# Kernel optimization log

Measured on AMD Instinct MI355X. Metric: run time of the kernel, lower is better.

The kernel has to match this reference:

```python
import jax, jax.numpy as jnp
import numpy as np

DIM = 64
WIDTH = 128
INPUT_DIM = 16
N_NODES = 50000
N_EDGES = 100000
N_GRAPHS = 2500
STEPS = 5


def setup_inputs() -> dict:
    key = jax.random.key(0)
    ks = jax.random.split(key, 24)
    d = DIM
    def nrm(i, shape, fan_in):
        return jax.random.normal(ks[i], shape, jnp.float32) / np.float32(np.sqrt(fan_in))
    return {
        "x": jax.random.normal(ks[0], (N_NODES, INPUT_DIM - 1), jnp.float32),
        "z": jax.random.normal(ks[1], (N_NODES,), jnp.float32),
        "edge_attr": jax.random.uniform(ks[2], (N_EDGES, 5), jnp.float32),
        "lin0_w": nrm(3, (INPUT_DIM, d), INPUT_DIM),
        "lin0_b": jnp.zeros((d,), jnp.float32),
        "emlp_w1": nrm(4, (5, WIDTH), 5),
        "emlp_b1": jnp.zeros((WIDTH,), jnp.float32),
        "emlp_w2": nrm(5, (WIDTH, d * d), WIDTH),
        "emlp_b2": jnp.zeros((d * d,), jnp.float32),
        "conv_root": nrm(6, (d, d), d),
        "conv_bias": jnp.zeros((d,), jnp.float32),
        "gru_wi": nrm(7, (3 * d, d), d),
        "gru_wh": nrm(8, (3 * d, d), d),
        "gru_bi": jnp.zeros((3 * d,), jnp.float32),
        "gru_bh": jnp.zeros((3 * d,), jnp.float32),
        "lstm_wi": nrm(9, (4 * d, 2 * d), 2 * d),
        "lstm_wh": nrm(10, (4 * d, d), d),
        "lstm_bi": jnp.zeros((4 * d,), jnp.float32),
        "lstm_bh": jnp.zeros((4 * d,), jnp.float32),
        "lin1_w": nrm(11, (2 * d, d), 2 * d),
        "lin1_b": jnp.zeros((d,), jnp.float32),
        "lin2_w": nrm(12, (d, 1), d),
        "lin2_b": jnp.zeros((1,), jnp.float32),
        "edge_index": jax.random.randint(ks[13], (2, N_EDGES), 0, N_NODES),
        "batch": jnp.sort(jax.random.randint(ks[14], (N_NODES,), 0, N_GRAPHS)),
        "num_graphs": N_GRAPHS,
    }


def reference(x, z, edge_attr, lin0_w, lin0_b, emlp_w1, emlp_b1, emlp_w2, emlp_b2,
              conv_root, conv_bias, gru_wi, gru_wh, gru_bi, gru_bh,
              lstm_wi, lstm_wh, lstm_bi, lstm_bh, lin1_w, lin1_b, lin2_w, lin2_b,
              edge_index, batch, num_graphs):
    d = lin0_w.shape[1]
    n = x.shape[0]
    src, dst = edge_index[0], edge_index[1]
    # lin0 on [x | z]
    out = jax.nn.relu(jnp.concatenate([x, z[:, None]], axis=-1) @ lin0_w + lin0_b)  # [N, d]
    h = out
    # edge MLP -> per-edge weight matrix [E, d, d] (edge_attr fixed, compute once)
    ew = (jax.nn.relu(edge_attr @ emlp_w1 + emlp_b1) @ emlp_w2 + emlp_b2).reshape(-1, d, d)
    deg = jax.ops.segment_sum(jnp.ones_like(src, jnp.float32), dst, num_segments=n)
    denom = jnp.maximum(deg, 1.0)[:, None]
    for _ in range(STEPS):
        # NNConv: gather-matmul-scatter(mean) + root transform + bias
        msg = jnp.einsum('ei,eio->eo', out[src], ew)  # [E, d]
        aggr = jax.ops.segment_sum(msg, dst, num_segments=n) / denom
        m = jax.nn.relu(aggr + out @ conv_root + conv_bias)
        # GRU cell (torch gate order r, z, n)
        gi = m @ gru_wi.T + gru_bi
        gh = h @ gru_wh.T + gru_bh
        i_r, i_z, i_n = jnp.split(gi, 3, axis=-1)
        h_r, h_z, h_n = jnp.split(gh, 3, axis=-1)
        r = jax.nn.sigmoid(i_r + h_r)
        zg = jax.nn.sigmoid(i_z + h_z)
        ng = jnp.tanh(i_n + r * h_n)
        h = (1.0 - zg) * ng + zg * h
        out = h
    # Set2Set pooling (LSTM(2d -> d), torch gate order i, f, g, o)
    B = num_graphs
    q_star = jnp.zeros((B, 2 * d), out.dtype)
    hh = jnp.zeros((B, d), out.dtype)
    cc = jnp.zeros((B, d), out.dtype)
    for _ in range(STEPS):
        g = q_star @ lstm_wi.T + lstm_bi + hh @ lstm_wh.T + lstm_bh
        gi_, gf_, gg_, go_ = jnp.split(g, 4, axis=-1)
        cc = jax.nn.sigmoid(gf_) * cc + jax.nn.sigmoid(gi_) * jnp.tanh(gg_)
        hh = jax.nn.sigmoid(go_) * jnp.tanh(cc)
        q = hh
        e = jnp.sum(out * q[batch], axis=-1)  # [N]
        emax = jax.ops.segment_max(e, batch, num_segments=B)
        a = jnp.exp(e - emax[batch])
        asum = jax.ops.segment_sum(a, batch, num_segments=B) + 1e-16
        a = a / asum[batch]
        r_pool = jax.ops.segment_sum(a[:, None] * out, batch, num_segments=B)  # [B, d]
        q_star = jnp.concatenate([q, r_pool], axis=-1)
    y = jax.nn.relu(q_star @ lin1_w + lin1_b) @ lin2_w + lin2_b
    return y.reshape(-1)
```

## Files before the change

### kernel.cpp

```cpp
#include <hip/hip_runtime.h>
#include <hip/hip_bf16.h>

#define NN 50000
#define NE 100000
#define NG 2500
#define WW 128
#define EPAD 100096
#define KCH 264

typedef _Float16 h8 __attribute__((ext_vector_type(8)));
typedef _Float16 h4 __attribute__((ext_vector_type(4)));
typedef float    f4 __attribute__((ext_vector_type(4)));

#define GLOAD_LDS16(g, l) __builtin_amdgcn_global_load_lds( \
    (const __attribute__((address_space(1))) void*)(g),     \
    (__attribute__((address_space(3))) void*)(l), 16, 0, 0)

__device__ __forceinline__ float sigf(float x) { return 1.0f / (1.0f + __expf(-x)); }

__global__ void k_zero4(float4* __restrict__ p, int n4) {
    int i = blockIdx.x * 256 + threadIdx.x;
    if (i < n4) p[i] = make_float4(0.f, 0.f, 0.f, 0.f);
}

__global__ void k_transpose(float* dst, const float* src, int rows, int cols) {
    int idx = blockIdx.x * 256 + threadIdx.x;
    if (idx >= rows * cols) return;
    int r = idx / cols, c = idx % cols;
    dst[c * rows + r] = src[idx];
}

__global__ void k_lin0(const float* __restrict__ x, const float* __restrict__ z,
                       const float* __restrict__ w, const float* __restrict__ b,
                       float* __restrict__ s) {
    int idx = blockIdx.x * 256 + threadIdx.x;
    int n = idx >> 6, o = idx & 63;
    float acc = b[o];
#pragma unroll
    for (int i = 0; i < 15; i++) acc += x[n * 15 + i] * w[i * 64 + o];
    acc += z[n] * w[15 * 64 + o];
    s[idx] = fmaxf(acc, 0.0f);
}

__global__ void k_deg(const int* __restrict__ dstI, float* __restrict__ deg) {
    int e = blockIdx.x * 256 + threadIdx.x;
    if (e < NE) atomicAdd(&deg[dstI[e]], 1.0f);
}

__global__ void k_s16(const float* __restrict__ s, _Float16* __restrict__ s16) {
    int i = blockIdx.x * 256 + threadIdx.x;
    float4 v = ((const float4*)s)[i];
    h4 o = { (_Float16)v.x, (_Float16)v.y, (_Float16)v.z, (_Float16)v.w };
    *((h4*)s16 + i) = o;
}

__global__ void k_gstart(const int* __restrict__ batch, int* __restrict__ gstart) {
    int n = blockIdx.x * 256 + threadIdx.x;
    if (n > NN) return;
    int b1 = (n < NN) ? batch[n] : NG;
    int b0 = (n == 0) ? -1 : batch[n - 1];
    for (int g = b0 + 1; g <= b1; g++) gstart[g] = n;
}

__global__ void k_emlp_t(const float* __restrict__ ea, const float* __restrict__ w1,
                         const float* __restrict__ b1, _Float16* __restrict__ hidT4) {
    __shared__ _Float16 hl[132][64];
    int t = threadIdx.x;
    int e0 = blockIdx.x * 64;
    int e_l = t & 63, w = t >> 6;
    int e = e0 + e_l;
    float a0 = 0, a1 = 0, a2 = 0, a3 = 0, a4 = 0;
    if (e < NE) {
        a0 = ea[e * 5 + 0]; a1 = ea[e * 5 + 1]; a2 = ea[e * 5 + 2];
        a3 = ea[e * 5 + 3]; a4 = ea[e * 5 + 4];
    }
    for (int h = w * 32; h < w * 32 + 32; h++) {
        float acc = b1[h];
        acc += a0 * w1[0 * 128 + h] + a1 * w1[1 * 128 + h] + a2 * w1[2 * 128 + h]
             + a3 * w1[3 * 128 + h] + a4 * w1[4 * 128 + h];
        hl[h][e_l] = (_Float16)fmaxf(acc, 0.0f);
    }
    if (t < 64) hl[128][t] = (_Float16)1.0f;
    else if (t < 128) hl[129][t - 64] = (_Float16)0.0f;
    else if (t < 192) hl[130][t - 128] = (_Float16)0.0f;
    else hl[131][t - 192] = (_Float16)0.0f;
    __syncthreads();
#pragma unroll
    for (int it = 0; it < 9; it++) {
        int hq = it * 4 + w;
        if (hq < 33) {
            h4 v = { hl[hq * 4 + 0][e_l], hl[hq * 4 + 1][e_l],
                     hl[hq * 4 + 2][e_l], hl[hq * 4 + 3][e_l] };
            *(h4*)(hidT4 + ((size_t)hq * EPAD + e0 + e_l) * 4) = v;
        }
    }
}

__global__ void k_prep_B(const float* __restrict__ w2, const float* __restrict__ b2,
                         _Float16* __restrict__ Bp) {
    int g = blockIdx.x * 256 + threadIdx.x;
    int l = g & 63, tt = (g >> 6) & 3, c = g >> 8;
    int n = tt * 16 + (l & 15);
    int kb = c * 32 + (l >> 4) * 8;
    h8 v;
#pragma unroll
    for (int j = 0; j < 8; j++) {
        int k = kb + j;
        float f = 0.0f;
        if (k < 8192) f = w2[(size_t)k * 64 + n];
        else if (k < 8256) f = b2[(k - 8192) * 64 + n];
        v[j] = (_Float16)f;
    }
    *((h8*)Bp + g) = v;
}

__global__ void k_prep_W(const float* __restrict__ conv_root,
                         const float* __restrict__ gru_wi,
                         const float* __restrict__ gru_wh,
                         _Float16* __restrict__ Bw) {
    int g = blockIdx.x * 256 + threadIdx.x;
    if (g >= 56 * 64) return;
    int l = g & 63, unit = g >> 6;
    int kb = ((unit & 1) * 32) + (l >> 4) * 8;
    h8 v;
    if (unit < 8) {
        int nt = unit >> 1;
        int n = nt * 16 + (l & 15);
#pragma unroll
        for (int j = 0; j < 8; j++) v[j] = (_Float16)conv_root[(kb + j) * 64 + n];
    } else if (unit < 32) {
        int nt = (unit - 8) >> 1;
        int o = nt * 16 + (l & 15);
#pragma unroll
        for (int j = 0; j < 8; j++) v[j] = (_Float16)gru_wi[o * 64 + kb + j];
    } else {
        int nt = (unit - 32) >> 1;
        int o = nt * 16 + (l & 15);
#pragma unroll
        for (int j = 0; j < 8; j++) v[j] = (_Float16)gru_wh[o * 64 + kb + j];
    }
    *((h8*)Bw + g) = v;
}

#define COMPUTE_PHASE(BUF, PAIR)                                               \
    _Pragma("unroll")                                                          \
    for (int c2 = 0; c2 < 4; c2++) {                                           \
        h8 b0 = *(const h8*)&Bl[BUF][(c2 * 4 + 0) * 64 + lane];                \
        h8 b1 = *(const h8*)&Bl[BUF][(c2 * 4 + 1) * 64 + lane];                \
        h8 b2 = *(const h8*)&Bl[BUF][(c2 * 4 + 2) * 64 + lane];                \
        h8 b3 = *(const h8*)&Bl[BUF][(c2 * 4 + 3) * 64 + lane];                \
        _Pragma("unroll")                                                      \
        for (int mt = 0; mt < 4; mt++) {                                       \
            h8 a = sA[mt][c2 & 1] * hfA[mt][(PAIR) * 2 + (c2 >> 1)];           \
            acc[mt][0] = __builtin_amdgcn_mfma_f32_16x16x32_f16(a, b0, acc[mt][0], 0, 0, 0); \
            acc[mt][1] = __builtin_amdgcn_mfma_f32_16x16x32_f16(a, b1, acc[mt][1], 0, 0, 0); \
            acc[mt][2] = __builtin_amdgcn_mfma_f32_16x16x32_f16(a, b2, acc[mt][2], 0, 0, 0); \
            acc[mt][3] = __builtin_amdgcn_mfma_f32_16x16x32_f16(a, b3, acc[mt][3], 0, 0, 0); \
        }                                                                      \
    }

__global__ __launch_bounds__(128, 2) void k_fused(
        const _Float16* __restrict__ s16, const _Float16* __restrict__ hidT4,
        const _Float16* __restrict__ Bp, const int* __restrict__ srcI,
        const int* __restrict__ dstI, float* __restrict__ aggr) {
    __shared__ uint4 Bl[2][1024];
    int t = threadIdx.x, w = t >> 6, lane = t & 63;
    int m = lane & 15, q = lane >> 4;
    int e_blk = blockIdx.x * 128;
    int ew0 = e_blk + w * 64;

    h8 sA[4][2];
#pragma unroll
    for (int mt = 0; mt < 4; mt++) {
        int e = ew0 + mt * 16 + m;
        int src = (e < NE) ? srcI[e] : 0;
        const _Float16* sp = s16 + (size_t)src * 64;
        sA[mt][0] = *(const h8*)(sp + q * 8);
        sA[mt][1] = *(const h8*)(sp + 32 + q * 8);
    }
    f4 acc[4][4];
#pragma unroll
    for (int mt = 0; mt < 4; mt++)
#pragma unroll
        for (int nt = 0; nt < 4; nt++) acc[mt][nt] = (f4){0.f, 0.f, 0.f, 0.f};

    const h4* hT = (const h4*)hidT4;
    h4 hfA[4], hfB[4];
#pragma unroll
    for (int mt = 0; mt < 4; mt++)
        hfA[mt] = hT[(size_t)0 * EPAD + ew0 + mt * 16 + m];

    {
        const uint4* bs = (const uint4*)Bp;
#pragma unroll
        for (int r = 0; r < 8; r++) {
            int idx = r * 128 + t;
            GLOAD_LDS16(bs + idx, &Bl[0][idx]);
        }
    }
    __syncthreads();

    for (int tt = 0; tt < 33; tt++) {
        {
            const uint4* bs = (const uint4*)Bp + (size_t)(2 * tt + 1) * 1024;
#pragma unroll
            for (int r = 0; r < 8; r++) {
                int idx = r * 128 + t;
                GLOAD_LDS16(bs + idx, &Bl[1][idx]);
            }
        }
        if (tt + 1 < 33) {
#pragma unroll
            for (int mt = 0; mt < 4; mt++)
                hfB[mt] = hT[(size_t)(tt + 1) * EPAD + ew0 + mt * 16 + m];
        }
        COMPUTE_PHASE(0, 0)
        __syncthreads();

        if (tt + 1 < 33) {
            const uint4* bs = (const uint4*)Bp + (size_t)(2 * tt + 2) * 1024;
#pragma unroll
            for (int r = 0; r < 8; r++) {
                int idx = r * 128 + t;
                GLOAD_LDS16(bs + idx, &Bl[0][idx]);
            }
        }
        COMPUTE_PHASE(1, 1)
        if (tt + 1 < 33) {
#pragma unroll
            for (int mt = 0; mt < 4; mt++) hfA[mt] = hfB[mt];
        }
        __syncthreads();
    }

#pragma unroll
    for (int mt = 0; mt < 4; mt++) {
        int eb = ew0 + mt * 16 + q * 4;
#pragma unroll
        for (int r = 0; r < 4; r++) {
            int e = eb + r;
            if (e < NE) {
                int d = dstI[e];
                float* ap = aggr + (size_t)d * 64 + m;
                atomicAdd(ap + 0,  acc[mt][0][r]);
                atomicAdd(ap + 16, acc[mt][1][r]);
                atomicAdd(ap + 32, acc[mt][2][r]);
                atomicAdd(ap + 48, acc[mt][3][r]);
            }
        }
    }
}

__global__ __launch_bounds__(256) void k_combine2(
        float* __restrict__ s, _Float16* __restrict__ s16,
        const float* __restrict__ aggr, const float* __restrict__ deg,
        const _Float16* __restrict__ Bw, const float* __restrict__ cb,
        const float* __restrict__ bi, const float* __restrict__ bh) {
    __shared__ _Float16 ml[4][16][72];
    int t = threadIdx.x, w = t >> 6, lane = t & 63;
    int m = lane & 15, q = lane >> 4;
    int nb = blockIdx.x * 64 + w * 16;

    h8 sa0, sa1;
    {
        int node = nb + m; if (node >= NN) node = NN - 1;
        const _Float16* sp = s16 + (size_t)node * 64;
        sa0 = *(const h8*)(sp + q * 8);
        sa1 = *(const h8*)(sp + 32 + q * 8);
    }
    const h8* BW = (const h8*)Bw;

    f4 X[4], GH[12];
#pragma unroll
    for (int nt = 0; nt < 4; nt++) {
        X[nt] = (f4){0.f, 0.f, 0.f, 0.f};
        X[nt] = __builtin_amdgcn_mfma_f32_16x16x32_f16(sa0, BW[(nt * 2 + 0) * 64 + lane], X[nt], 0, 0, 0);
        X[nt] = __builtin_amdgcn_mfma_f32_16x16x32_f16(sa1, BW[(nt * 2 + 1) * 64 + lane], X[nt], 0, 0, 0);
    }
#pragma unroll
    for (int nt = 0; nt < 12; nt++) {
        GH[nt] = (f4){0.f, 0.f, 0.f, 0.f};
        GH[nt] = __builtin_amdgcn_mfma_f32_16x16x32_f16(sa0, BW[(32 + nt * 2 + 0) * 64 + lane], GH[nt], 0, 0, 0);
        GH[nt] = __builtin_amdgcn_mfma_f32_16x16x32_f16(sa1, BW[(32 + nt * 2 + 1) * 64 + lane], GH[nt], 0, 0, 0);
    }
#pragma unroll
    for (int r = 0; r < 4; r++) {
        int node = nb + q * 4 + r; if (node >= NN) node = NN - 1;
        float dn = fmaxf(deg[node], 1.0f);
#pragma unroll
        for (int nt = 0; nt < 4; nt++) {
            int o = nt * 16 + m;
            float mv = X[nt][r] + aggr[(size_t)node * 64 + o] / dn + cb[o];
            ml[w][q * 4 + r][o] = (_Float16)fmaxf(mv, 0.0f);
        }
    }
    __syncthreads();
    h8 ma0 = *(const h8*)&ml[w][m][q * 8];
    h8 ma1 = *(const h8*)&ml[w][m][32 + q * 8];

    f4 GI[12];
#pragma unroll
    for (int nt = 0; nt < 12; nt++) {
        GI[nt] = (f4){0.f, 0.f, 0.f, 0.f};
        GI[nt] = __builtin_amdgcn_mfma_f32_16x16x32_f16(ma0, BW[(8 + nt * 2 + 0) * 64 + lane], GI[nt], 0, 0, 0);
        GI[nt] = __builtin_amdgcn_mfma_f32_16x16x32_f16(ma1, BW[(8 + nt * 2 + 1) * 64 + lane], GI[nt], 0, 0, 0);
    }
#pragma unroll
    for (int og = 0; og < 4; og++) {
        int o = og * 16 + m;
        float bir = bi[o],       bhr = bh[o];
        float biz = bi[64 + o],  bhz = bh[64 + o];
        float bin = bi[128 + o], bhn = bh[128 + o];
#pragma unroll
        for (int r = 0; r < 4; r++) {
            int node = nb + q * 4 + r;
            if (node >= NN) continue;
            float rr = sigf(GI[og][r] + bir + GH[og][r] + bhr);
            float zz = sigf(GI[4 + og][r] + biz + GH[4 + og][r] + bhz);
            float ng = tanhf(GI[8 + og][r] + bin + rr * (GH[8 + og][r] + bhn));
            float hold = s[(size_t)node * 64 + o];
            float hnew = (1.0f - zz) * ng + zz * hold;
            s[(size_t)node * 64 + o] = hnew;
            s16[(size_t)node * 64 + o] = (_Float16)hnew;
        }
    }
}

__global__ void k_s2s(float* __restrict__ q_star, float* __restrict__ hh,
                      float* __restrict__ cc, const float* __restrict__ LiT,
                      const float* __restrict__ LhT, const float* __restrict__ bi,
                      const float* __restrict__ bh, const float* __restrict__ s,
                      const int* __restrict__ gstart, float* __restrict__ e_v) {
    __shared__ float qs[128], hv[64], g[256], qn[64];
    int b = blockIdx.x, t = threadIdx.x;
    if (t < 128) qs[t] = q_star[b * 128 + t];
    else if (t < 192) hv[t - 128] = hh[b * 64 + t - 128];
    __syncthreads();
    float acc = bi[t] + bh[t];
    for (int k = 0; k < 128; k++) acc += qs[k] * LiT[k * 256 + t];
    for (int k = 0; k < 64; k++) acc += hv[k] * LhT[k * 256 + t];
    g[t] = acc;
    __syncthreads();
    if (t < 64) {
        float c_new = sigf(g[64 + t]) * cc[b * 64 + t] + sigf(g[t]) * tanhf(g[128 + t]);
        cc[b * 64 + t] = c_new;
        float hq = sigf(g[192 + t]) * tanhf(c_new);
        hh[b * 64 + t] = hq;
        qn[t] = hq;
        q_star[b * 128 + t] = hq;
    }
    __syncthreads();
    if (t >= 64) return;
    int o = t;
    int n0 = gstart[b], n1 = gstart[b + 1];
    float q = qn[o];
    float mx = -3.4e38f;
    for (int n = n0; n < n1; n++) {
        float v = s[(size_t)n * 64 + o] * q;
#pragma unroll
        for (int off = 32; off; off >>= 1) v += __shfl_xor(v, off, 64);
        if (o == 0) e_v[n] = v;
        mx = fmaxf(mx, v);
    }
    float asum = 0.0f, rp = 0.0f;
    for (int n = n0; n < n1; n++) {
        float a = __expf(e_v[n] - mx);
        asum += a;
        rp += a * s[(size_t)n * 64 + o];
    }
    q_star[b * 128 + 64 + o] = rp / (asum + 1e-16f);
}

__global__ void k_final(const float* __restrict__ q_star, const float* __restrict__ w1,
                        const float* __restrict__ b1, const float* __restrict__ w2,
                        const float* __restrict__ b2, float* __restrict__ y) {
    __shared__ float qs[128];
    int b = blockIdx.x, t = threadIdx.x;
    qs[t] = q_star[b * 128 + t];
    qs[64 + t] = q_star[b * 128 + 64 + t];
    __syncthreads();
    float acc = b1[t];
    for (int k = 0; k < 128; k++) acc += qs[k] * w1[k * 64 + t];
    float hid = fmaxf(acc, 0.0f) * w2[t];
#pragma unroll
    for (int off = 32; off; off >>= 1) hid += __shfl_down(hid, off, 64);
    if (t == 0) y[b] = hid + b2[0];
}

static inline void zero_f(float* p, size_t nfloats, hipStream_t stream) {
    int n4 = (int)(nfloats / 4);
    k_zero4<<<(n4 + 255) / 256, 256, 0, stream>>>((float4*)p, n4);
}

extern "C" void kernel_launch(void* const* d_in, const int* in_sizes, int n_in,
                              void* d_out, int out_size, void* d_ws, size_t ws_size,
                              hipStream_t stream) {
    const float* x       = (const float*)d_in[0];
    const float* z       = (const float*)d_in[1];
    const float* ea      = (const float*)d_in[2];
    const float* lin0_w  = (const float*)d_in[3];
    const float* lin0_b  = (const float*)d_in[4];
    const float* emlp_w1 = (const float*)d_in[5];
    const float* emlp_b1 = (const float*)d_in[6];
    const float* emlp_w2 = (const float*)d_in[7];
    const float* emlp_b2 = (const float*)d_in[8];
    const float* conv_r  = (const float*)d_in[9];
    const float* conv_b  = (const float*)d_in[10];
    const float* gru_wi  = (const float*)d_in[11];
    const float* gru_wh  = (const float*)d_in[12];
    const float* gru_bi  = (const float*)d_in[13];
    const float* gru_bh  = (const float*)d_in[14];
    const float* lstm_wi = (const float*)d_in[15];
    const float* lstm_wh = (const float*)d_in[16];
    const float* lstm_bi = (const float*)d_in[17];
    const float* lstm_bh = (const float*)d_in[18];
    const float* lin1_w  = (const float*)d_in[19];
    const float* lin1_b  = (const float*)d_in[20];
    const float* lin2_w  = (const float*)d_in[21];
    const float* lin2_b  = (const float*)d_in[22];
    const int* eidx      = (const int*)d_in[23];
    const int* batch     = (const int*)d_in[24];
    const int* srcI = eidx;
    const int* dstI = eidx + NE;
    float* y = (float*)d_out;

    char* w = (char*)d_ws;
    size_t off = 0;
    auto alloc = [&](size_t bytes) -> void* {
        void* p = w + off;
        off += (bytes + 255) & ~(size_t)255;
        return p;
    };
    float* s      = (float*)alloc((size_t)NN * 64 * 4);
    float* aggr   = (float*)alloc((size_t)NN * 64 * 4);
    float* deg    = (float*)alloc((size_t)NN * 4);
    float* e_v    = (float*)alloc((size_t)NN * 4);
    float* q_star = (float*)alloc((size_t)NG * 128 * 4);
    float* hh     = (float*)alloc((size_t)NG * 64 * 4);
    float* cc     = (float*)alloc((size_t)NG * 64 * 4);
    float* LiT    = (float*)alloc(256 * 128 * 4);
    float* LhT    = (float*)alloc(256 * 64 * 4);
    int*   gstart = (int*)alloc((size_t)(NG + 1) * 4);
    _Float16* s16 = (_Float16*)alloc((size_t)NN * 64 * 2);
    _Float16* hidT= (_Float16*)alloc((size_t)33 * EPAD * 4 * 2);
    _Float16* Bp  = (_Float16*)alloc((size_t)KCH * 4 * 64 * 8 * 2);
    _Float16* Bw  = (_Float16*)alloc((size_t)56 * 64 * 8 * 2);
    (void)ws_size;

    k_transpose<<<(256 * 128 + 255) / 256, 256, 0, stream>>>(LiT, lstm_wi, 256, 128);
    k_transpose<<<(256 * 64 + 255) / 256, 256, 0, stream>>>(LhT, lstm_wh, 256, 64);
    k_prep_W<<<14, 256, 0, stream>>>(conv_r, gru_wi, gru_wh, Bw);

    k_lin0<<<NN * 64 / 256, 256, 0, stream>>>(x, z, lin0_w, lin0_b, s);
    k_s16<<<NN * 16 / 256, 256, 0, stream>>>(s, s16);
    zero_f(deg, NN, stream);
    k_deg<<<(NE + 255) / 256, 256, 0, stream>>>(dstI, deg);
    k_gstart<<<(NN + 256) / 256, 256, 0, stream>>>(batch, gstart);
    k_emlp_t<<<EPAD / 64, 256, 0, stream>>>(ea, emlp_w1, emlp_b1, hidT);
    k_prep_B<<<KCH * 4 * 64 / 256, 256, 0, stream>>>(emlp_w2, emlp_b2, Bp);

    for (int step = 0; step < 5; step++) {
        zero_f(aggr, (size_t)NN * 64, stream);
        k_fused<<<EPAD / 128, 128, 0, stream>>>(s16, hidT, Bp, srcI, dstI, aggr);
        k_combine2<<<(NN + 63) / 64, 256, 0, stream>>>(s, s16, aggr, deg, Bw,
                                                       conv_b, gru_bi, gru_bh);
    }

    zero_f(q_star, (size_t)NG * 128 + NG * 64 + NG * 64, stream);
    for (int it = 0; it < 5; it++) {
        k_s2s<<<NG, 256, 0, stream>>>(q_star, hh, cc, LiT, LhT, lstm_bi, lstm_bh,
                                      s, gstart, e_v);
    }
    k_final<<<NG, 64, 0, stream>>>(q_star, lin1_w, lin1_b, lin2_w, lin2_b, y);
}
```

Baseline: 1.095 ms.

## Split fused edge GEMM by output half, load B directly into registers

The fused edge-message kernel now runs one wave per block. Each block handles 128 edges (8 m-tiles) and one of two output-column halves, selected by blockIdx.y. The B operand is read straight from global memory into registers with a software prefetch, replacing the LDS double buffer and its barriers. This doubles per-wave edge reuse of each B fragment but recomputes the A scaling and gathers for both halves. The loop also prefetches one chunk past the end without a guard, so the hidT and Bp allocations are padded to keep those reads in bounds.

```diff
diff --git a/kernel.cpp b/kernel.cpp
--- a/kernel.cpp
+++ b/kernel.cpp
@@ -11,10 +11,6 @@
 typedef _Float16 h8 __attribute__((ext_vector_type(8)));
 typedef _Float16 h4 __attribute__((ext_vector_type(4)));
 typedef float    f4 __attribute__((ext_vector_type(4)));
-
-#define GLOAD_LDS16(g, l) __builtin_amdgcn_global_load_lds( \
-    (const __attribute__((address_space(1))) void*)(g),     \
-    (__attribute__((address_space(3))) void*)(l), 16, 0, 0)
 
 __device__ __forceinline__ float sigf(float x) { return 1.0f / (1.0f + __expf(-x)); }
 
@@ -142,110 +138,94 @@
     *((h8*)Bw + g) = v;
 }
 
-#define COMPUTE_PHASE(BUF, PAIR)                                               \
-    _Pragma("unroll")                                                          \
-    for (int c2 = 0; c2 < 4; c2++) {                                           \
-        h8 b0 = *(const h8*)&Bl[BUF][(c2 * 4 + 0) * 64 + lane];                \
-        h8 b1 = *(const h8*)&Bl[BUF][(c2 * 4 + 1) * 64 + lane];                \
-        h8 b2 = *(const h8*)&Bl[BUF][(c2 * 4 + 2) * 64 + lane];                \
-        h8 b3 = *(const h8*)&Bl[BUF][(c2 * 4 + 3) * 64 + lane];                \
-        _Pragma("unroll")                                                      \
-        for (int mt = 0; mt < 4; mt++) {                                       \
-            h8 a = sA[mt][c2 & 1] * hfA[mt][(PAIR) * 2 + (c2 >> 1)];           \
-            acc[mt][0] = __builtin_amdgcn_mfma_f32_16x16x32_f16(a, b0, acc[mt][0], 0, 0, 0); \
-            acc[mt][1] = __builtin_amdgcn_mfma_f32_16x16x32_f16(a, b1, acc[mt][1], 0, 0, 0); \
-            acc[mt][2] = __builtin_amdgcn_mfma_f32_16x16x32_f16(a, b2, acc[mt][2], 0, 0, 0); \
-            acc[mt][3] = __builtin_amdgcn_mfma_f32_16x16x32_f16(a, b3, acc[mt][3], 0, 0, 0); \
-        }                                                                      \
-    }
-
-__global__ __launch_bounds__(128, 2) void k_fused(
+__global__ __launch_bounds__(64, 2) void k_fused(
         const _Float16* __restrict__ s16, const _Float16* __restrict__ hidT4,
         const _Float16* __restrict__ Bp, const int* __restrict__ srcI,
         const int* __restrict__ dstI, float* __restrict__ aggr) {
-    __shared__ uint4 Bl[2][1024];
-    int t = threadIdx.x, w = t >> 6, lane = t & 63;
+    int lane = threadIdx.x;
     int m = lane & 15, q = lane >> 4;
     int e_blk = blockIdx.x * 128;
-    int ew0 = e_blk + w * 64;
-
-    h8 sA[4][2];
-#pragma unroll
-    for (int mt = 0; mt < 4; mt++) {
-        int e = ew0 + mt * 16 + m;
+    int nh = blockIdx.y;
+
+    h8 sA0[8], sA1[8];
+#pragma unroll
+    for (int mt = 0; mt < 8; mt++) {
+        int e = e_blk + mt * 16 + m;
         int src = (e < NE) ? srcI[e] : 0;
         const _Float16* sp = s16 + (size_t)src * 64;
-        sA[mt][0] = *(const h8*)(sp + q * 8);
-        sA[mt][1] = *(const h8*)(sp + 32 + q * 8);
-    }
-    f4 acc[4][4];
-#pragma unroll
-    for (int mt = 0; mt < 4; mt++)
-#pragma unroll
-        for (int nt = 0; nt < 4; nt++) acc[mt][nt] = (f4){0.f, 0.f, 0.f, 0.f};
+        sA0[mt] = *(const h8*)(sp + q * 8);
+        sA1[mt] = *(const h8*)(sp + 32 + q * 8);
+    }
+    f4 acc[8][2];
+#pragma unroll
+    for (int mt = 0; mt < 8; mt++) {
+        acc[mt][0] = (f4){0.f, 0.f, 0.f, 0.f};
+        acc[mt][1] = (f4){0.f, 0.f, 0.f, 0.f};
+    }
 
     const h4* hT = (const h4*)hidT4;
-    h4 hfA[4], hfB[4];
-#pragma unroll
-    for (int mt = 0; mt < 4; mt++)
-        hfA[mt] = hT[(size_t)0 * EPAD + ew0 + mt * 16 + m];
-
-    {
-        const uint4* bs = (const uint4*)Bp;
-#pragma unroll
-        for (int r = 0; r < 8; r++) {
-            int idx = r * 128 + t;
-            GLOAD_LDS16(bs + idx, &Bl[0][idx]);
-        }
-    }
-    __syncthreads();
+    h4 hfA[8], hfB[8];
+#pragma unroll
+    for (int mt = 0; mt < 8; mt++)
+        hfA[mt] = hT[(size_t)0 * EPAD + e_blk + mt * 16 + m];
+
+    const h8* Bbase = (const h8*)Bp + (size_t)nh * 2 * 64 + lane;
+
+    h8 Bc[8], Bn[8];
+#pragma unroll
+    for (int f = 0; f < 8; f++) {
+        int c2 = f >> 1, nt = f & 1;
+        Bc[f] = Bbase[(c2 * 4 + nt) * 64];
+    }
 
     for (int tt = 0; tt < 33; tt++) {
-        {
-            const uint4* bs = (const uint4*)Bp + (size_t)(2 * tt + 1) * 1024;
-#pragma unroll
-            for (int r = 0; r < 8; r++) {
-                int idx = r * 128 + t;
-                GLOAD_LDS16(bs + idx, &Bl[1][idx]);
+        int ck0 = tt * 8;
+#pragma unroll
+        for (int f = 0; f < 8; f++) {
+            int c2 = f >> 1, nt = f & 1;
+            Bn[f] = Bbase[((ck0 + 4 + c2) * 4 + nt) * 64];
+        }
+#pragma unroll
+        for (int mt = 0; mt < 8; mt++)
+            hfB[mt] = hT[(size_t)(tt + 1) * EPAD + e_blk + mt * 16 + m];
+#pragma unroll
+        for (int c2 = 0; c2 < 4; c2++) {
+#pragma unroll
+            for (int mt = 0; mt < 8; mt++) {
+                h8 a = (c2 & 1 ? sA1[mt] : sA0[mt]) * hfA[mt][c2 >> 1];
+                acc[mt][0] = __builtin_amdgcn_mfma_f32_16x16x32_f16(a, Bc[c2 * 2 + 0], acc[mt][0], 0, 0, 0);
+                acc[mt][1] = __builtin_amdgcn_mfma_f32_16x16x32_f16(a, Bc[c2 * 2 + 1], acc[mt][1], 0, 0, 0);
             }
         }
-        if (tt + 1 < 33) {
-#pragma unroll
-            for (int mt = 0; mt < 4; mt++)
-                hfB[mt] = hT[(size_t)(tt + 1) * EPAD + ew0 + mt * 16 + m];
-        }
-        COMPUTE_PHASE(0, 0)
-        __syncthreads();
-
-        if (tt + 1 < 33) {
-            const uint4* bs = (const uint4*)Bp + (size_t)(2 * tt + 2) * 1024;
-#pragma unroll
-            for (int r = 0; r < 8; r++) {
-                int idx = r * 128 + t;
-                GLOAD_LDS16(bs + idx, &Bl[0][idx]);
+#pragma unroll
+        for (int f = 0; f < 8; f++) {
+            int c2 = f >> 1, nt = f & 1;
+            Bc[f] = Bbase[((ck0 + 8 + c2) * 4 + nt) * 64];
+        }
+#pragma unroll
+        for (int c2 = 0; c2 < 4; c2++) {
+#pragma unroll
+            for (int mt = 0; mt < 8; mt++) {
+                h8 a = (c2 & 1 ? sA1[mt] : sA0[mt]) * hfA[mt][2 + (c2 >> 1)];
+                acc[mt][0] = __builtin_amdgcn_mfma_f32_16x16x32_f16(a, Bn[c2 * 2 + 0], acc[mt][0], 0, 0, 0);
+                acc[mt][1] = __builtin_amdgcn_mfma_f32_16x16x32_f16(a, Bn[c2 * 2 + 1], acc[mt][1], 0, 0, 0);
             }
         }
-        COMPUTE_PHASE(1, 1)
-        if (tt + 1 < 33) {
-#pragma unroll
-            for (int mt = 0; mt < 4; mt++) hfA[mt] = hfB[mt];
-        }
-        __syncthreads();
-    }
-
-#pragma unroll
-    for (int mt = 0; mt < 4; mt++) {
-        int eb = ew0 + mt * 16 + q * 4;
+#pragma unroll
+        for (int mt = 0; mt < 8; mt++) hfA[mt] = hfB[mt];
+    }
+
+#pragma unroll
+    for (int mt = 0; mt < 8; mt++) {
+        int eb = e_blk + mt * 16 + q * 4;
 #pragma unroll
         for (int r = 0; r < 4; r++) {
             int e = eb + r;
             if (e < NE) {
                 int d = dstI[e];
-                float* ap = aggr + (size_t)d * 64 + m;
+                float* ap = aggr + (size_t)d * 64 + nh * 32 + m;
                 atomicAdd(ap + 0,  acc[mt][0][r]);
                 atomicAdd(ap + 16, acc[mt][1][r]);
-                atomicAdd(ap + 32, acc[mt][2][r]);
-                atomicAdd(ap + 48, acc[mt][3][r]);
             }
         }
     }
@@ -442,8 +422,8 @@
     float* LhT    = (float*)alloc(256 * 64 * 4);
     int*   gstart = (int*)alloc((size_t)(NG + 1) * 4);
     _Float16* s16 = (_Float16*)alloc((size_t)NN * 64 * 2);
-    _Float16* hidT= (_Float16*)alloc((size_t)33 * EPAD * 4 * 2);
-    _Float16* Bp  = (_Float16*)alloc((size_t)KCH * 4 * 64 * 8 * 2);
+    _Float16* hidT= (_Float16*)alloc((size_t)34 * EPAD * 4 * 2);
+    _Float16* Bp  = (_Float16*)alloc((size_t)(KCH + 4) * 4 * 64 * 8 * 2);
     _Float16* Bw  = (_Float16*)alloc((size_t)56 * 64 * 8 * 2);
     (void)ws_size;
 
@@ -461,7 +441,7 @@
 
     for (int step = 0; step < 5; step++) {
         zero_f(aggr, (size_t)NN * 64, stream);
-        k_fused<<<EPAD / 128, 128, 0, stream>>>(s16, hidT, Bp, srcI, dstI, aggr);
+        k_fused<<<dim3(EPAD / 128, 2), 64, 0, stream>>>(s16, hidT, Bp, srcI, dstI, aggr);
         k_combine2<<<(NN + 63) / 64, 256, 0, stream>>>(s, s16, aggr, deg, Bw,
                                                        conv_b, gru_bi, gru_bh);
     }
```

Result: no change. 1.096 ms (+0.1%).
